# Kernel optimization log

Measured on AMD Instinct MI355X. Metric: run time of the kernel, lower is better.

## Reference

```python
import jax, jax.numpy as jnp
import numpy as np

D = 128          # state dimension d
H = 256          # nabla_V MLP hidden width
NUM_STEPS = 300  # Euler-Maruyama steps
B = 512          # batch of trajectories
T_FINAL = 1.0
LMBD = 1.0


def _mlp(tx, W1, b1, W2, b2):
    # neural_sde.nabla_V : (N, D+1) -> (N, D)
    return jnp.tanh(tx @ W1 + b1) @ W2 + b2


def setup_inputs() -> dict:
    key = jax.random.key(0)
    ks = jax.random.split(key, 8)
    x0 = jax.random.normal(ks[0], (D,), jnp.float32)
    sigma = jnp.eye(D, dtype=jnp.float32)                      # default sigma = I
    A = 0.05 * jax.random.normal(ks[1], (D, D), jnp.float32) - jnp.eye(D)  # stable linear drift b(x)=Ax
    Mp = jax.random.normal(ks[2], (D, D), jnp.float32)
    P = 0.1 * (Mp @ Mp.T) / D
    Mq = jax.random.normal(ks[3], (D, D), jnp.float32)
    Q = 0.1 * (Mq @ Mq.T) / D
    W1 = jax.random.normal(ks[4], (D + 1, H), jnp.float32) / np.sqrt(D + 1)
    b1 = jnp.zeros((H,), jnp.float32)
    W2 = jax.random.normal(ks[5], (H, D), jnp.float32) / np.sqrt(H)
    b2 = jnp.zeros((D,), jnp.float32)
    noises = jax.random.normal(ks[6], (NUM_STEPS, B, D), jnp.float32)  # unit normals
    return dict(x0=x0, sigma=sigma, A=A, P=P, Q=Q, W1=W1, b1=b1, W2=W2, b2=b2, noises=noises)


def reference(x0, sigma, A, P, Q, W1, b1, W2, b2, noises):
    # SOC_Solver.loss(batch_size=B, algorithm='SOCM_const_M')
    ts = jnp.linspace(0.0, T_FINAL, NUM_STEPS + 1)
    dts = ts[1:] - ts[:-1]
    state0 = jnp.broadcast_to(x0, (B, D))

    # ---- utils.stochastic_trajectories: Euler-Maruyama rollout with log-weight accumulation ----
    def step(carry, inp):
        x, lw_det, lw_sto = carry
        t0, dt, noise = inp
        tx = jnp.concatenate([jnp.full((B, 1), t0, x.dtype), x], axis=-1)
        nv = _mlp(tx, W1, b1, W2, b2)
        u = jax.lax.stop_gradient(-nv @ sigma)  # control = -sigma^T nabla_V, detached (SOCM)
        f_val = 0.5 * jnp.einsum('bi,ij,bj->b', x, P, x)
        x_new = x + (x @ A.T + u @ sigma.T) * dt + jnp.sqrt(LMBD * dt) * (noise @ sigma.T)
        lw_det = lw_det + dt * (-0.5 * jnp.sum(u * u, -1) / LMBD - f_val / LMBD)
        lw_sto = lw_sto + jnp.sqrt(dt / LMBD) * jnp.sum(u * noise, -1)
        return (x_new, lw_det, lw_sto), (x_new, u)

    init = (state0, jnp.zeros((B,), state0.dtype), jnp.zeros((B,), state0.dtype))
    (xT, lw_det, lw_sto), (xs, controls) = jax.lax.scan(step, init, (ts[:-1], dts, noises))
    states = jnp.concatenate([state0[None], xs], 0)               # (T+1, B, D)
    log_terminal = -0.5 * jnp.einsum('bi,ij,bj->b', xT, Q, xT) / LMBD
    weight = jnp.exp(lw_det + lw_sto + log_terminal)              # (B,)

    # ---- nabla_V over the whole trajectory ----
    ts_rep = jnp.broadcast_to(ts[:, None, None], (NUM_STEPS + 1, B, 1))
    tx_all = jnp.concatenate([ts_rep, states], -1).reshape(-1, D + 1)
    nabla_V = _mlp(tx_all, W1, b1, W2, b2).reshape(NUM_STEPS + 1, B, D)

    # ---- SOCM_const_M least-squares target ----
    sigma_inv_T = jnp.linalg.inv(sigma).T
    term1 = jnp.einsum('ij,tbj->tbi', P, states[:-1])             # nabla_f(states)[:-1]
    sin_noises = jnp.einsum('ij,tbj->tbi', sigma_inv_T, noises)
    sin_controls = jnp.einsum('ij,tbj->tbi', sigma_inv_T, controls)
    term2 = -jnp.sqrt(LMBD) * jnp.einsum('ij,tbj->tbi', A, sin_noises)   # nabla_b == A (const)
    term3 = -jnp.einsum('ij,tbj->tbi', A, sin_controls)
    target_terminal = states[-1] @ Q.T                            # nabla_g(x_T)

    dt_b = dts[:, None, None]
    z = jnp.zeros((1, B, D), states.dtype)
    t1dt = jnp.concatenate([z, term1 * dt_b], 0)
    t2sdt = jnp.concatenate([z, term2 * jnp.sqrt(dt_b)], 0)
    t3dt = jnp.concatenate([z, term3 * dt_b], 0)
    cs1 = jnp.sum(t1dt, 0, keepdims=True) - jnp.cumsum(t1dt, 0)
    cs2 = jnp.sum(t2sdt, 0, keepdims=True) - jnp.cumsum(t2sdt, 0)
    cs3 = jnp.sum(t3dt, 0, keepdims=True) - jnp.cumsum(t3dt, 0)
    least_squares_target = cs1 + cs2 + cs3 + target_terminal[None]

    control_learned = -jnp.einsum('ij,tbj->tbi', sigma.T, nabla_V)
    control_target = -jnp.einsum('ij,tbj->tbi', sigma.T, least_squares_target)
    w = weight[None, :, None]
    objective = jnp.sum((control_learned - control_target) ** 2 * w) / ((NUM_STEPS + 1) * B)
    return objective
```

## Files before the change

kernel.cpp:

```cpp
#include <hip/hip_runtime.h>
#include <math.h>

#define DD 128
#define HH 256
#define NS 300
#define BB 512
#define NPO (301*64)

__device__ __forceinline__ float tsf(int t){ return (float)((double)t*(1.0/(double)NS)); }

__device__ __forceinline__ float wave_red(float v){
#pragma unroll
  for(int o=32;o>0;o>>=1) v += __shfl_down(v,o);
  return v;
}
__device__ __forceinline__ float fma4(float4 a, float4 b, float acc){
  acc = fmaf(a.x,b.x,acc); acc = fmaf(a.y,b.y,acc);
  acc = fmaf(a.z,b.z,acc); acc = fmaf(a.w,b.w,acc); return acc;
}

__global__ __launch_bounds__(256) void k_pre1(
    const float* __restrict__ sigma,
    float* __restrict__ SIT, float* __restrict__ AUG, int* __restrict__ FLG)
{
  const int j = threadIdx.x;
  __shared__ int s_ok; __shared__ int s_p; __shared__ float s_fac[DD];
  if (j == 0) s_ok = 1;
  __syncthreads();
  bool ok = true;
  for (int idx = j; idx < DD*DD; idx += 256) {
    const int r = idx >> 7, c = idx & 127;
    if (sigma[idx] != (r==c ? 1.f : 0.f)) ok = false;
  }
  if (!ok) s_ok = 0;
  __syncthreads();
  const bool ident = (s_ok != 0);
  if (j == 0) *FLG = ident ? 1 : 0;
  if (ident) {
    for (int idx = j; idx < DD*DD; idx += 256) {
      const int r = idx >> 7, c = idx & 127;
      SIT[idx] = (r==c) ? 1.f : 0.f;
    }
    return;
  }
  for (int idx = j; idx < DD*256; idx += 256) {
    const int r = idx >> 8, c = idx & 255;
    AUG[idx] = (c < DD) ? sigma[r*DD + c] : ((c-DD)==r ? 1.f : 0.f);
  }
  __syncthreads();
  for (int c = 0; c < DD; ++c) {
    if (j == 0) {
      int p = c; float best = fabsf(AUG[c*256 + c]);
      for (int r2 = c+1; r2 < DD; ++r2) {
        const float v = fabsf(AUG[r2*256 + c]);
        if (v > best) { best = v; p = r2; }
      }
      s_p = p;
    }
    __syncthreads();
    const int p = s_p;
    if (p != c) {
      const float tmp = AUG[c*256 + j];
      AUG[c*256 + j] = AUG[p*256 + j];
      AUG[p*256 + j] = tmp;
    }
    __syncthreads();
    const float pd = AUG[c*256 + c];
    const float rowv = AUG[c*256 + j];
    __syncthreads();
    AUG[c*256 + j] = rowv / pd;
    if (j < DD) s_fac[j] = (j == c) ? 0.f : AUG[j*256 + c];
    __syncthreads();
    const float prj = AUG[c*256 + j];
    for (int r2 = 0; r2 < DD; ++r2) {
      if (r2 != c) AUG[r2*256 + j] -= s_fac[r2] * prj;
    }
    __syncthreads();
  }
  for (int idx = j; idx < DD*DD; idx += 256) {
    const int j2 = idx >> 7, k = idx & 127;
    SIT[idx] = AUG[k*256 + DD + j2];
  }
}

__global__ __launch_bounds__(256) void k_pre2(
    const float* __restrict__ W1, const float* __restrict__ W2,
    const float* __restrict__ A, const float* __restrict__ P,
    const float* __restrict__ Q, const float* __restrict__ sigma,
    const float* __restrict__ SIT, const int* __restrict__ FLG,
    float* __restrict__ W1L, float* __restrict__ W2L,
    float* __restrict__ AL, float* __restrict__ PL,
    float* __restrict__ ML, float* __restrict__ SL,
    float* __restrict__ STL, float* __restrict__ QL,
    float* __restrict__ SGC)
{
  const int g = blockIdx.x*256 + threadIdx.x;
  const int gs = gridDim.x*256;
  const bool ident = (*FLG != 0);
  for (int idx = g; idx < 32*256; idx += gs) {
    const int k4 = idx >> 8, hj = idx & 255;
#pragma unroll
    for (int j = 0; j < 4; ++j)
      W1L[idx*4 + j] = W1[(4*k4 + 1 + j)*HH + hj];
  }
  for (int idx = g; idx < 64*128; idx += gs) {
    const int k4 = idx >> 7, i = idx & 127;
#pragma unroll
    for (int j = 0; j < 4; ++j)
      W2L[idx*4 + j] = W2[(4*k4 + j)*DD + i];
  }
  for (int idx = g; idx < 32*128; idx += gs) {
    const int k4 = idx >> 7, i = idx & 127;
#pragma unroll
    for (int j = 0; j < 4; ++j) {
      AL [idx*4 + j] = A[i*DD + 4*k4 + j];
      PL [idx*4 + j] = P[i*DD + 4*k4 + j];
      QL [idx*4 + j] = Q[i*DD + 4*k4 + j];
      STL[idx*4 + j] = sigma[i*DD + 4*k4 + j];
      SL [idx*4 + j] = sigma[(4*k4 + j)*DD + i];
      float m;
      if (ident) m = -A[i*DD + 4*k4 + j];
      else {
        float acc = 0.f;
        for (int jj = 0; jj < DD; ++jj)
          acc = fmaf(A[i*DD + jj], SIT[jj*DD + 4*k4 + j], acc);
        m = -acc;
      }
      ML[idx*4 + j] = m;
    }
  }
  for (int idx = g; idx < DD*DD; idx += gs) {
    const int i2 = idx >> 7, k = idx & 127;
    SGC[idx] = sigma[k*DD + i2];
  }
}

__global__ __launch_bounds__(512) void k_roll_id4(
    const float* __restrict__ x0,
    const float* __restrict__ W1, const float* __restrict__ b1,
    const float* __restrict__ b2, const float* __restrict__ noises,
    const float* __restrict__ W1L, const float* __restrict__ W2L,
    const float* __restrict__ AL, const float* __restrict__ PL,
    const float* __restrict__ QL, const int* __restrict__ FLG,
    float* __restrict__ U, float* __restrict__ TL,
    float* __restrict__ TGT, float* __restrict__ WGT)
{
  if (*FLG == 0) return;
  __shared__ __align__(16) float xs[4][128];
  __shared__ __align__(16) float hs[4][256];
  __shared__ __align__(16) float wv[4][128];
  __shared__ __align__(16) float p2[2][4][256];
  __shared__ __align__(16) float p4[4][4][128];
  __shared__ __align__(16) float pm3[3][4][4][128];
  __shared__ float red[16];

  const float4* W1L4 = (const float4*)W1L;
  const float4* W2L4 = (const float4*)W2L;
  const float4* AL4  = (const float4*)AL;
  const float4* PL4  = (const float4*)PL;
  const float4* QL4  = (const float4*)QL;
  float4* xs4 = (float4*)&xs[0][0];
  float4* hs4 = (float4*)&hs[0][0];
  float4* wv4 = (float4*)&wv[0][0];
  float* p4f = &p4[0][0][0];
  float* pA  = &pm3[0][0][0][0];
  float* pP  = &pm3[1][0][0][0];
  float* pM  = &pm3[2][0][0][0];

  const int tid = threadIdx.x;
  const int hj = tid & 255, hg = tid >> 8;
  const int i  = tid & 127, q  = tid >> 7;
  const int wid = tid >> 6;
  const int b0 = blockIdx.x * 4;
  const float w1t = (hg == 0) ? W1[hj] : 0.f;
  const float b1c = b1[hj];
  const float b2i = b2[i];

  xs[q][i] = x0[i];

  float lwloc = 0.f, u_reg = 0.f, nz = 0.f;

  for (int t = 0; t <= NS; ++t) {
    __syncthreads();
    const float t0 = tsf(t);
    const float dt = tsf(t+1) - t0;
    const float sdt = sqrtf(dt);
    nz = (t < NS) ? noises[((size_t)t*BB + b0 + q)*DD + i] : 0.f;

    {
      float a0 = t0*w1t, a1 = t0*w1t, a2 = t0*w1t, a3 = t0*w1t;
#pragma unroll
      for (int m = 0; m < 16; ++m) {
        const float4 w = W1L4[(hg*16 + m)*256 + hj];
        a0 = fma4(w, xs4[0*32 + hg*16 + m], a0);
        a1 = fma4(w, xs4[1*32 + hg*16 + m], a1);
        a2 = fma4(w, xs4[2*32 + hg*16 + m], a2);
        a3 = fma4(w, xs4[3*32 + hg*16 + m], a3);
      }
      p2[hg][0][hj] = a0; p2[hg][1][hj] = a1;
      p2[hg][2][hj] = a2; p2[hg][3][hj] = a3;
    }
    __syncthreads();
    {
      const int rr = tid >> 8, cc = tid & 255;
      hs[rr][cc]     = tanhf(p2[0][rr][cc]     + p2[1][rr][cc]     + b1c);
      hs[rr + 2][cc] = tanhf(p2[0][rr + 2][cc] + p2[1][rr + 2][cc] + b1c);
    }
    __syncthreads();
    {
      float c0 = 0.f, c1 = 0.f, c2 = 0.f, c3 = 0.f;
#pragma unroll
      for (int m = 0; m < 16; ++m) {
        const float4 w2 = W2L4[(q*16 + m)*128 + i];
        c0 = fma4(w2, hs4[0*64 + q*16 + m], c0);
        c1 = fma4(w2, hs4[1*64 + q*16 + m], c1);
        c2 = fma4(w2, hs4[2*64 + q*16 + m], c2);
        c3 = fma4(w2, hs4[3*64 + q*16 + m], c3);
      }
      p4f[q*512 + 0*128 + i] = c0; p4f[q*512 + 1*128 + i] = c1;
      p4f[q*512 + 2*128 + i] = c2; p4f[q*512 + 3*128 + i] = c3;
    }
    __syncthreads();
    {
      const float nv = p4f[0*512 + q*128 + i] + p4f[1*512 + q*128 + i]
                     + p4f[2*512 + q*128 + i] + p4f[3*512 + q*128 + i] + b2i;
      u_reg = -nv;
      U[((size_t)t*BB + b0 + q)*DD + i] = u_reg;
      if (t < NS) {
        wv[q][i] = sdt*nz + dt*u_reg;
        lwloc += sdt*u_reg*nz - 0.5f*dt*u_reg*u_reg;
      }
    }
    if (t == NS) break;
    __syncthreads();
    {
      float aA[4] = {0,0,0,0}, aP_[4] = {0,0,0,0}, aM[4] = {0,0,0,0};
#pragma unroll
      for (int m = 0; m < 8; ++m) {
        const float4 av = AL4[(q*8 + m)*128 + i];
        const float4 pv = PL4[(q*8 + m)*128 + i];
#pragma unroll
        for (int r = 0; r < 4; ++r) {
          const float4 xv = xs4[r*32 + q*8 + m];
          const float4 wvv = wv4[r*32 + q*8 + m];
          aA[r] = fma4(av, xv, aA[r]);
          aP_[r] = fma4(pv, xv, aP_[r]);
          aM[r] = fma4(av, wvv, aM[r]);
        }
      }
#pragma unroll
      for (int r = 0; r < 4; ++r) {
        pA[q*512 + r*128 + i] = aA[r];
        pP[q*512 + r*128 + i] = aP_[r];
        pM[q*512 + r*128 + i] = aM[r];
      }
    }
    __syncthreads();
    {
      const float xo = xs[q][i];
      const float xa = pA[0*512 + q*128 + i] + pA[1*512 + q*128 + i]
                     + pA[2*512 + q*128 + i] + pA[3*512 + q*128 + i];
      const float yy = pP[0*512 + q*128 + i] + pP[1*512 + q*128 + i]
                     + pP[2*512 + q*128 + i] + pP[3*512 + q*128 + i];
      const float mm = -(pM[0*512 + q*128 + i] + pM[1*512 + q*128 + i]
                       + pM[2*512 + q*128 + i] + pM[3*512 + q*128 + i]);
      TL[(size_t)(t+1)*(BB*DD) + (size_t)(b0 + q)*DD + i] = dt*yy + mm;
      xs[q][i] = xo + (xa + u_reg)*dt + sdt*nz;
      lwloc -= 0.5f*dt*xo*yy;
    }
  }
  __syncthreads();
  {
    float g0 = 0.f, g1 = 0.f, g2 = 0.f, g3 = 0.f;
#pragma unroll
    for (int m = 0; m < 8; ++m) {
      const float4 qv = QL4[(q*8 + m)*128 + i];
      g0 = fma4(qv, xs4[0*32 + q*8 + m], g0);
      g1 = fma4(qv, xs4[1*32 + q*8 + m], g1);
      g2 = fma4(qv, xs4[2*32 + q*8 + m], g2);
      g3 = fma4(qv, xs4[3*32 + q*8 + m], g3);
    }
    pA[q*512 + 0*128 + i] = g0; pA[q*512 + 1*128 + i] = g1;
    pA[q*512 + 2*128 + i] = g2; pA[q*512 + 3*128 + i] = g3;
  }
  __syncthreads();
  float qloc;
  {
    const float tt = pA[0*512 + q*128 + i] + pA[1*512 + q*128 + i]
                   + pA[2*512 + q*128 + i] + pA[3*512 + q*128 + i];
    TGT[(b0 + q)*DD + i] = tt;
    qloc = xs[q][i]*tt;
  }
  const float rq = wave_red(qloc);
  const float rl = wave_red(lwloc);
  if ((tid & 63) == 0) { red[wid] = rq; red[8 + wid] = rl; }
  __syncthreads();
  if (tid < 4) {
    const float qf = red[2*tid] + red[2*tid + 1];
    const float lw = red[8 + 2*tid] + red[8 + 2*tid + 1];
    WGT[b0 + tid] = expf(lw - 0.5f*qf);
  }
}

__global__ __launch_bounds__(512) void k_roll_gen(
    const float* __restrict__ x0,
    const float* __restrict__ W1, const float* __restrict__ b1,
    const float* __restrict__ b2, const float* __restrict__ noises,
    const float* __restrict__ W1L, const float* __restrict__ W2L,
    const float* __restrict__ AL, const float* __restrict__ PL,
    const float* __restrict__ ML, const float* __restrict__ SL,
    const float* __restrict__ STL, const float* __restrict__ QL,
    const int* __restrict__ FLG,
    float* __restrict__ U, float* __restrict__ TL,
    float* __restrict__ TGT, float* __restrict__ WGT)
{
  if (*FLG != 0) return;
  __shared__ __align__(16) float xs[2][128];
  __shared__ __align__(16) float hs[2][256];
  __shared__ __align__(16) float noi[2][128];
  __shared__ __align__(16) float nvs[2][128];
  __shared__ __align__(16) float uu[2][128];
  __shared__ __align__(16) float wv[2][128];
  __shared__ __align__(16) float p2[2][2][256];
  __shared__ __align__(16) float p4[4][2][128];
  __shared__ __align__(16) float pm3[3][4][2][128];
  __shared__ float red[16];

  const float4* W1L4 = (const float4*)W1L;
  const float4* W2L4 = (const float4*)W2L;
  const float4* AL4  = (const float4*)AL;
  const float4* PL4  = (const float4*)PL;
  const float4* ML4  = (const float4*)ML;
  const float4* SL4  = (const float4*)SL;
  const float4* STL4 = (const float4*)STL;
  const float4* QL4  = (const float4*)QL;
  float4* xs4  = (float4*)&xs[0][0];
  float4* hs4  = (float4*)&hs[0][0];
  float4* wv4  = (float4*)&wv[0][0];
  float4* nvs4 = (float4*)&nvs[0][0];
  float4* uu4  = (float4*)&uu[0][0];
  float4* noi4 = (float4*)&noi[0][0];
  float* p2f = &p2[0][0][0];
  float* p4f = &p4[0][0][0];
  float* pA  = &pm3[0][0][0][0];
  float* pP  = &pm3[1][0][0][0];
  float* pM  = &pm3[2][0][0][0];

  const int tid = threadIdx.x;
  const int hj = tid & 255, hg = tid >> 8;
  const int i  = tid & 127, q  = tid >> 7;
  const int wid = tid >> 6;
  const int b0 = blockIdx.x * 2;
  const float w1t = (hg == 0) ? W1[hj] : 0.f;
  const float b1c = b1[hj];
  const float b2i = b2[i];

  if (tid < 256) xs[tid >> 7][tid & 127] = x0[tid & 127];

  float lwloc = 0.f, u_reg = 0.f, nz = 0.f;

  for (int t = 0; t <= NS; ++t) {
    __syncthreads();
    const float t0 = tsf(t);
    const float dt = tsf(t+1) - t0;
    const float sdt = sqrtf(dt);
    nz = 0.f;
    if (q < 2 && t < NS) {
      nz = noises[((size_t)t*BB + b0 + q)*DD + i];
      noi[q][i] = nz;
    }
    {
      float a0 = t0*w1t, a1 = t0*w1t;
#pragma unroll
      for (int m = 0; m < 16; ++m) {
        const float4 w = W1L4[(hg*16 + m)*256 + hj];
        a0 = fma4(w, xs4[hg*16 + m], a0);
        a1 = fma4(w, xs4[32 + hg*16 + m], a1);
      }
      p2[hg][0][hj] = a0; p2[hg][1][hj] = a1;
    }
    __syncthreads();
    {
      const int rr = tid >> 8, cc = tid & 255;
      hs[rr][cc] = tanhf(p2[0][rr][cc] + p2[1][rr][cc] + b1c);
    }
    __syncthreads();
    {
      float c0 = 0.f, c1 = 0.f;
#pragma unroll
      for (int m = 0; m < 16; ++m) {
        const float4 w2 = W2L4[(q*16 + m)*128 + i];
        c0 = fma4(w2, hs4[q*16 + m], c0);
        c1 = fma4(w2, hs4[64 + q*16 + m], c1);
      }
      p4[q][0][i] = c0; p4[q][1][i] = c1;
    }
    __syncthreads();
    if (q < 2) {
      nvs[q][i] = p4[0][q][i] + p4[1][q][i] + p4[2][q][i] + p4[3][q][i] + b2i;
    }
    __syncthreads();
    {
      float s0 = 0.f, s1 = 0.f;
#pragma unroll
      for (int m = 0; m < 8; ++m) {
        const float4 gv = SL4[(q*8 + m)*128 + i];
        s0 = fma4(gv, nvs4[q*8 + m], s0);
        s1 = fma4(gv, nvs4[32 + q*8 + m], s1);
      }
      pA[q*256 + i] = s0; pA[q*256 + 128 + i] = s1;
    }
    __syncthreads();
    if (q < 2) {
      u_reg = -(pA[q*128 + i] + pA[256 + q*128 + i]
              + pA[512 + q*128 + i] + pA[768 + q*128 + i]);
      uu[q][i] = u_reg;
      U[((size_t)t*BB + b0 + q)*DD + i] = u_reg;
      wv[q][i] = sdt*nz + dt*u_reg;
      if (t < NS) lwloc += sdt*u_reg*nz - 0.5f*dt*u_reg*u_reg;
    }
    if (t == NS) break;
    __syncthreads();
    {
      float aA0=0,aA1=0,aP0=0,aP1=0,aM0=0,aM1=0;
#pragma unroll
      for (int m = 0; m < 8; ++m) {
        const float4 av = AL4[(q*8 + m)*128 + i];
        const float4 pv = PL4[(q*8 + m)*128 + i];
        const float4 mv = ML4[(q*8 + m)*128 + i];
        const float4 x0v = xs4[q*8 + m];
        const float4 x1v = xs4[32 + q*8 + m];
        const float4 w0v = wv4[q*8 + m];
        const float4 w1v = wv4[32 + q*8 + m];
        aA0 = fma4(av, x0v, aA0); aA1 = fma4(av, x1v, aA1);
        aP0 = fma4(pv, x0v, aP0); aP1 = fma4(pv, x1v, aP1);
        aM0 = fma4(mv, w0v, aM0); aM1 = fma4(mv, w1v, aM1);
      }
      pA[q*256 + i] = aA0; pA[q*256 + 128 + i] = aA1;
      pP[q*256 + i] = aP0; pP[q*256 + 128 + i] = aP1;
      pM[q*256 + i] = aM0; pM[q*256 + 128 + i] = aM1;
      float su0=0,su1=0,sn0=0,sn1=0;
#pragma unroll
      for (int m = 0; m < 8; ++m) {
        const float4 sv = STL4[(q*8 + m)*128 + i];
        su0 = fma4(sv, uu4[q*8 + m],  su0);
        su1 = fma4(sv, uu4[32 + q*8 + m], su1);
        sn0 = fma4(sv, noi4[q*8 + m], sn0);
        sn1 = fma4(sv, noi4[32 + q*8 + m], sn1);
      }
      p2f[q*256 + i] = su0; p2f[q*256 + 128 + i] = su1;
      p4f[q*256 + i] = sn0; p4f[q*256 + 128 + i] = sn1;
    }
    __syncthreads();
    if (q < 2) {
      const float xo = xs[q][i];
      const float xa = pA[q*128+i] + pA[256+q*128+i] + pA[512+q*128+i] + pA[768+q*128+i];
      const float yy = pP[q*128+i] + pP[256+q*128+i] + pP[512+q*128+i] + pP[768+q*128+i];
      const float mm = pM[q*128+i] + pM[256+q*128+i] + pM[512+q*128+i] + pM[768+q*128+i];
      const float usv = p2f[q*128+i] + p2f[256+q*128+i] + p2f[512+q*128+i] + p2f[768+q*128+i];
      const float nsv = p4f[q*128+i] + p4f[256+q*128+i] + p4f[512+q*128+i] + p4f[768+q*128+i];
      TL[(size_t)(t+1)*(BB*DD) + (size_t)(b0 + q)*DD + i] = dt*yy + mm;
      xs[q][i] = xo + (xa + usv)*dt + sdt*nsv;
      lwloc -= 0.5f*dt*xo*yy;
    }
  }
  __syncthreads();
  {
    float g0 = 0.f, g1 = 0.f;
#pragma unroll
    for (int m = 0; m < 8; ++m) {
      const float4 qv = QL4[(q*8 + m)*128 + i];
      g0 = fma4(qv, xs4[q*8 + m], g0);
      g1 = fma4(qv, xs4[32 + q*8 + m], g1);
    }
    pA[q*256 + i] = g0; pA[q*256 + 128 + i] = g1;
  }
  __syncthreads();
  float qloc = 0.f;
  if (q < 2) {
    const float tt = pA[q*128+i] + pA[256+q*128+i] + pA[512+q*128+i] + pA[768+q*128+i];
    TGT[(b0 + q)*DD + i] = tt;
    qloc = xs[q][i]*tt;
  }
  const float rq = wave_red(qloc);
  const float rl = wave_red(lwloc);
  if ((tid & 63) == 0) { red[wid] = rq; red[8 + wid] = rl; }
  __syncthreads();
  if (tid < 2) {
    const float qf = red[2*tid] + red[2*tid + 1];
    const float lw = red[8 + 2*tid] + red[8 + 2*tid + 1];
    WGT[b0 + tid] = expf(lw - 0.5f*qf);
  }
}

__global__ __launch_bounds__(256) void k_scan(
    const float* __restrict__ TGT, const float* __restrict__ WGT,
    const float* __restrict__ U, float* __restrict__ TL,
    const int* __restrict__ FLG, float* __restrict__ PART_S)
{
  const int tid = threadIdx.x;
  const int bi = blockIdx.x*256 + tid;
  const int b = bi >> 7;
  const bool id = (*FLG != 0);
  const float w = WGT[b];
  float lst = TGT[bi];
  float obj = 0.f;
  if (id) { const float d = lst + U[(size_t)NS*(BB*DD) + bi]; obj = w*d*d; }
#pragma unroll 4
  for (int t = NS; t >= 1; --t) {
    const float v = TL[(size_t)t*(BB*DD) + bi];
    if (!id) TL[(size_t)t*(BB*DD) + bi] = lst;
    lst += v;
    if (id) { const float d = lst + U[(size_t)(t-1)*(BB*DD) + bi]; obj += w*d*d; }
  }
  if (!id) TL[bi] = lst;
  __shared__ float r4[4];
  const float s = wave_red(obj);
  if ((tid & 63) == 0) r4[tid >> 6] = s;
  __syncthreads();
  if (tid == 0) PART_S[blockIdx.x] = id ? (r4[0]+r4[1]+r4[2]+r4[3]) : 0.f;
}

__global__ __launch_bounds__(256) void k_obj(
    const float* __restrict__ SGC, const float* __restrict__ TL,
    const float* __restrict__ U, const float* __restrict__ WGT,
    const int* __restrict__ FLG, float* __restrict__ PART_O)
{
  const int blk = blockIdx.x;
  if (*FLG != 0) { if (threadIdx.x == 0) PART_O[blk] = 0.f; return; }
  const int t = blk >> 6, bg = blk & 63;
  __shared__ __align__(16) float ls[8][132];
  __shared__ __align__(16) float us[8][128];
  __shared__ __align__(16) float pD[2][8][128];
  __shared__ float wg[8];
  __shared__ float r4[4];
  const int tid = threadIdx.x;
  const int i = tid & 127, h = tid >> 7;
  for (int idx = tid; idx < 8*128; idx += 256) {
    const int rr = idx >> 7, k = idx & 127;
    ls[rr][k] = TL[(size_t)t*(BB*DD) + (size_t)(bg*8+rr)*DD + k];
    us[rr][k] = U [(size_t)t*(BB*DD) + (size_t)(bg*8+rr)*DD + k];
  }
  if (tid < 8) wg[tid] = WGT[bg*8 + tid];
  __syncthreads();
  const float* grow = SGC + i*DD + h*64;
#pragma unroll
  for (int rr = 0; rr < 8; ++rr) {
    float a = 0.f;
#pragma unroll
    for (int it = 0; it < 16; ++it) {
      float4 gv = *(const float4*)(grow + it*4);
      float4 l4 = *(const float4*)&ls[rr][h*64 + it*4];
      a = fma4(gv, l4, a);
    }
    pD[h][rr][i] = a;
  }
  __syncthreads();
  float obj = 0.f;
#pragma unroll
  for (int p = 0; p < 4; ++p) {
    const int rr = h*4 + p;
    const float d = pD[0][rr][i] + pD[1][rr][i] + us[rr][i];
    obj += wg[rr]*d*d;
  }
  const float s = wave_red(obj);
  if ((tid & 63) == 0) r4[tid >> 6] = s;
  __syncthreads();
  if (tid == 0) PART_O[blk] = r4[0]+r4[1]+r4[2]+r4[3];
}

__global__ __launch_bounds__(256) void k_fin(
    const float* __restrict__ PART_S, const float* __restrict__ PART_O,
    float* __restrict__ out)
{
  const int tid = threadIdx.x;
  float s = PART_S[tid];
  for (int idx = tid; idx < NPO; idx += 256) s += PART_O[idx];
  __shared__ float r4[4];
  const float v = wave_red(s);
  if ((tid & 63) == 0) r4[tid >> 6] = v;
  __syncthreads();
  if (tid == 0) out[0] = (r4[0]+r4[1]+r4[2]+r4[3]) * (1.0f/((float)(NS+1)*(float)BB));
}

extern "C" void kernel_launch(void* const* d_in, const int* in_sizes, int n_in,
                              void* d_out, int out_size, void* d_ws, size_t ws_size,
                              hipStream_t stream) {
  (void)in_sizes; (void)n_in; (void)out_size; (void)ws_size;
  const float* x0     = (const float*)d_in[0];
  const float* sigma  = (const float*)d_in[1];
  const float* A      = (const float*)d_in[2];
  const float* P      = (const float*)d_in[3];
  const float* Q      = (const float*)d_in[4];
  const float* W1     = (const float*)d_in[5];
  const float* b1     = (const float*)d_in[6];
  const float* W2     = (const float*)d_in[7];
  const float* b2     = (const float*)d_in[8];
  const float* noises = (const float*)d_in[9];

  float* ws = (float*)d_ws;
  const size_t SL_ = (size_t)BB*DD;
  float* TL     = ws;
  float* U      = TL + (size_t)(NS+1)*SL_;
  float* TGT    = U  + (size_t)(NS+1)*SL_;
  float* WGT    = TGT + SL_;
  float* W1Lw   = WGT + BB;
  float* W2Lw   = W1Lw + 32*256*4;
  float* ALm    = W2Lw + 64*128*4;
  float* PLm    = ALm + 32*128*4;
  float* MLm    = PLm + 32*128*4;
  float* SLm    = MLm + 32*128*4;
  float* STLm   = SLm + 32*128*4;
  float* QLm    = STLm + 32*128*4;
  float* SGC    = QLm + 32*128*4;
  float* SIT    = SGC + (size_t)DD*DD;
  float* AUG    = SIT + (size_t)DD*DD;
  float* PART_S = AUG + (size_t)DD*256;
  float* PART_O = PART_S + 256;
  int*   FLG    = (int*)(PART_O + NPO);
  float* out    = (float*)d_out;

  k_pre1<<<1, 256, 0, stream>>>(sigma, SIT, AUG, FLG);
  k_pre2<<<64, 256, 0, stream>>>(W1, W2, A, P, Q, sigma, SIT, FLG,
                                 W1Lw, W2Lw, ALm, PLm, MLm, SLm, STLm, QLm, SGC);
  k_roll_id4<<<128, 512, 0, stream>>>(x0, W1, b1, b2, noises,
                                      W1Lw, W2Lw, ALm, PLm, QLm, FLG,
                                      U, TL, TGT, WGT);
  k_roll_gen<<<256, 512, 0, stream>>>(x0, W1, b1, b2, noises,
                                      W1Lw, W2Lw, ALm, PLm, MLm, SLm, STLm, QLm,
                                      FLG, U, TL, TGT, WGT);
  k_scan<<<(BB*DD)/256, 256, 0, stream>>>(TGT, WGT, U, TL, FLG, PART_S);
  k_obj<<<NPO, 256, 0, stream>>>(SGC, TL, U, WGT, FLG, PART_O);
  k_fin<<<1, 256, 0, stream>>>(PART_S, PART_O, out);
}
```

Baseline: 1.821 ms.

## Process eight trajectories per block in identity-sigma rollout kernel

After: 4.591 ms. 2.52x slower.

```diff
diff --git a/kernel.cpp b/kernel.cpp
--- a/kernel.cpp
+++ b/kernel.cpp
@@ -6,6 +6,16 @@
 #define NS 300
 #define BB 512
 #define NPO (301*64)
+
+#define I8_XS   0
+#define I8_HS   1024
+#define I8_WV   3072
+#define I8_P2   4096
+#define I8_P4   8192
+#define I8_PM3  12288
+#define I8_RED  24576
+#define I8_FLOATS 24608
+#define I8_BYTES (I8_FLOATS*4)
 
 __device__ __forceinline__ float tsf(int t){ return (float)((double)t*(1.0/(double)NS)); }
 
@@ -135,7 +145,7 @@
   }
 }
 
-__global__ __launch_bounds__(512) void k_roll_id4(
+__global__ __launch_bounds__(512) void k_roll_id8(
     const float* __restrict__ x0,
     const float* __restrict__ W1, const float* __restrict__ b1,
     const float* __restrict__ b2, const float* __restrict__ noises,
@@ -146,159 +156,198 @@
     float* __restrict__ TGT, float* __restrict__ WGT)
 {
   if (*FLG == 0) return;
-  __shared__ __align__(16) float xs[4][128];
-  __shared__ __align__(16) float hs[4][256];
-  __shared__ __align__(16) float wv[4][128];
-  __shared__ __align__(16) float p2[2][4][256];
-  __shared__ __align__(16) float p4[4][4][128];
-  __shared__ __align__(16) float pm3[3][4][4][128];
-  __shared__ float red[16];
-
+  extern __shared__ float sm[];
+  float*  xs  = sm + I8_XS;
+  float*  hs  = sm + I8_HS;
+  float*  wv  = sm + I8_WV;
+  float*  p2  = sm + I8_P2;
+  float*  p4f = sm + I8_P4;
+  float*  pm3 = sm + I8_PM3;
+  float*  red = sm + I8_RED;
+  float4* xs4 = (float4*)xs;
+  float4* hs4 = (float4*)hs;
+  float4* wv4 = (float4*)wv;
+  float*  pA = pm3, *pP = pm3 + 4096, *pM = pm3 + 8192;
   const float4* W1L4 = (const float4*)W1L;
   const float4* W2L4 = (const float4*)W2L;
   const float4* AL4  = (const float4*)AL;
   const float4* PL4  = (const float4*)PL;
   const float4* QL4  = (const float4*)QL;
-  float4* xs4 = (float4*)&xs[0][0];
-  float4* hs4 = (float4*)&hs[0][0];
-  float4* wv4 = (float4*)&wv[0][0];
-  float* p4f = &p4[0][0][0];
-  float* pA  = &pm3[0][0][0][0];
-  float* pP  = &pm3[1][0][0][0];
-  float* pM  = &pm3[2][0][0][0];
 
   const int tid = threadIdx.x;
   const int hj = tid & 255, hg = tid >> 8;
   const int i  = tid & 127, q  = tid >> 7;
   const int wid = tid >> 6;
-  const int b0 = blockIdx.x * 4;
+  const int b0 = blockIdx.x * 8;
   const float w1t = (hg == 0) ? W1[hj] : 0.f;
   const float b1c = b1[hj];
   const float b2i = b2[i];
 
-  xs[q][i] = x0[i];
-
-  float lwloc = 0.f, u_reg = 0.f, nz = 0.f;
+  xs[q*128 + i] = x0[i];
+  xs[(q + 4)*128 + i] = x0[i];
+
+  float lw0 = 0.f, lw1 = 0.f;
+  float u0 = 0.f, u1 = 0.f, nz0 = 0.f, nz1 = 0.f;
 
   for (int t = 0; t <= NS; ++t) {
     __syncthreads();
     const float t0 = tsf(t);
     const float dt = tsf(t+1) - t0;
     const float sdt = sqrtf(dt);
-    nz = (t < NS) ? noises[((size_t)t*BB + b0 + q)*DD + i] : 0.f;
-
-    {
-      float a0 = t0*w1t, a1 = t0*w1t, a2 = t0*w1t, a3 = t0*w1t;
+    if (t < NS) {
+      nz0 = noises[((size_t)t*BB + b0 + q)*DD + i];
+      nz1 = noises[((size_t)t*BB + b0 + q + 4)*DD + i];
+    } else { nz0 = 0.f; nz1 = 0.f; }
+
+    {
+      float a[8];
+#pragma unroll
+      for (int r = 0; r < 8; ++r) a[r] = t0*w1t;
 #pragma unroll
       for (int m = 0; m < 16; ++m) {
         const float4 w = W1L4[(hg*16 + m)*256 + hj];
-        a0 = fma4(w, xs4[0*32 + hg*16 + m], a0);
-        a1 = fma4(w, xs4[1*32 + hg*16 + m], a1);
-        a2 = fma4(w, xs4[2*32 + hg*16 + m], a2);
-        a3 = fma4(w, xs4[3*32 + hg*16 + m], a3);
-      }
-      p2[hg][0][hj] = a0; p2[hg][1][hj] = a1;
-      p2[hg][2][hj] = a2; p2[hg][3][hj] = a3;
-    }
-    __syncthreads();
-    {
-      const int rr = tid >> 8, cc = tid & 255;
-      hs[rr][cc]     = tanhf(p2[0][rr][cc]     + p2[1][rr][cc]     + b1c);
-      hs[rr + 2][cc] = tanhf(p2[0][rr + 2][cc] + p2[1][rr + 2][cc] + b1c);
-    }
-    __syncthreads();
-    {
-      float c0 = 0.f, c1 = 0.f, c2 = 0.f, c3 = 0.f;
+#pragma unroll
+        for (int r = 0; r < 8; ++r)
+          a[r] = fma4(w, xs4[r*32 + hg*16 + m], a[r]);
+      }
+#pragma unroll
+      for (int r = 0; r < 8; ++r) p2[hg*2048 + r*256 + hj] = a[r];
+    }
+    __syncthreads();
+    {
+#pragma unroll
+      for (int rr = 0; rr < 4; ++rr) {
+        const int r = hg + rr*2;
+        hs[r*256 + hj] = tanhf(p2[r*256 + hj] + p2[2048 + r*256 + hj] + b1c);
+      }
+    }
+    __syncthreads();
+    {
+      float c[8];
+#pragma unroll
+      for (int r = 0; r < 8; ++r) c[r] = 0.f;
 #pragma unroll
       for (int m = 0; m < 16; ++m) {
         const float4 w2 = W2L4[(q*16 + m)*128 + i];
-        c0 = fma4(w2, hs4[0*64 + q*16 + m], c0);
-        c1 = fma4(w2, hs4[1*64 + q*16 + m], c1);
-        c2 = fma4(w2, hs4[2*64 + q*16 + m], c2);
-        c3 = fma4(w2, hs4[3*64 + q*16 + m], c3);
-      }
-      p4f[q*512 + 0*128 + i] = c0; p4f[q*512 + 1*128 + i] = c1;
-      p4f[q*512 + 2*128 + i] = c2; p4f[q*512 + 3*128 + i] = c3;
-    }
-    __syncthreads();
-    {
-      const float nv = p4f[0*512 + q*128 + i] + p4f[1*512 + q*128 + i]
-                     + p4f[2*512 + q*128 + i] + p4f[3*512 + q*128 + i] + b2i;
-      u_reg = -nv;
-      U[((size_t)t*BB + b0 + q)*DD + i] = u_reg;
+#pragma unroll
+        for (int r = 0; r < 8; ++r)
+          c[r] = fma4(w2, hs4[r*64 + q*16 + m], c[r]);
+      }
+#pragma unroll
+      for (int r = 0; r < 8; ++r) p4f[q*1024 + r*128 + i] = c[r];
+    }
+    __syncthreads();
+    {
+      const int r0 = q, r1 = q + 4;
+      const float nv0 = p4f[0*1024 + r0*128 + i] + p4f[1*1024 + r0*128 + i]
+                      + p4f[2*1024 + r0*128 + i] + p4f[3*1024 + r0*128 + i] + b2i;
+      const float nv1 = p4f[0*1024 + r1*128 + i] + p4f[1*1024 + r1*128 + i]
+                      + p4f[2*1024 + r1*128 + i] + p4f[3*1024 + r1*128 + i] + b2i;
+      u0 = -nv0; u1 = -nv1;
+      U[((size_t)t*BB + b0 + r0)*DD + i] = u0;
+      U[((size_t)t*BB + b0 + r1)*DD + i] = u1;
       if (t < NS) {
-        wv[q][i] = sdt*nz + dt*u_reg;
-        lwloc += sdt*u_reg*nz - 0.5f*dt*u_reg*u_reg;
+        wv[r0*128 + i] = sdt*nz0 + dt*u0;
+        wv[r1*128 + i] = sdt*nz1 + dt*u1;
+        lw0 += sdt*u0*nz0 - 0.5f*dt*u0*u0;
+        lw1 += sdt*u1*nz1 - 0.5f*dt*u1*u1;
       }
     }
     if (t == NS) break;
     __syncthreads();
     {
-      float aA[4] = {0,0,0,0}, aP_[4] = {0,0,0,0}, aM[4] = {0,0,0,0};
+      float aA[8], aP_[8], aM[8];
+#pragma unroll
+      for (int r = 0; r < 8; ++r) { aA[r] = 0.f; aP_[r] = 0.f; aM[r] = 0.f; }
 #pragma unroll
       for (int m = 0; m < 8; ++m) {
         const float4 av = AL4[(q*8 + m)*128 + i];
         const float4 pv = PL4[(q*8 + m)*128 + i];
 #pragma unroll
-        for (int r = 0; r < 4; ++r) {
-          const float4 xv = xs4[r*32 + q*8 + m];
+        for (int r = 0; r < 8; ++r) {
+          const float4 xv  = xs4[r*32 + q*8 + m];
           const float4 wvv = wv4[r*32 + q*8 + m];
-          aA[r] = fma4(av, xv, aA[r]);
+          aA[r]  = fma4(av, xv, aA[r]);
           aP_[r] = fma4(pv, xv, aP_[r]);
-          aM[r] = fma4(av, wvv, aM[r]);
+          aM[r]  = fma4(av, wvv, aM[r]);
         }
       }
 #pragma unroll
-      for (int r = 0; r < 4; ++r) {
-        pA[q*512 + r*128 + i] = aA[r];
-        pP[q*512 + r*128 + i] = aP_[r];
-        pM[q*512 + r*128 + i] = aM[r];
-      }
-    }
-    __syncthreads();
-    {
-      const float xo = xs[q][i];
-      const float xa = pA[0*512 + q*128 + i] + pA[1*512 + q*128 + i]
-                     + pA[2*512 + q*128 + i] + pA[3*512 + q*128 + i];
-      const float yy = pP[0*512 + q*128 + i] + pP[1*512 + q*128 + i]
-                     + pP[2*512 + q*128 + i] + pP[3*512 + q*128 + i];
-      const float mm = -(pM[0*512 + q*128 + i] + pM[1*512 + q*128 + i]
-                       + pM[2*512 + q*128 + i] + pM[3*512 + q*128 + i]);
-      TL[(size_t)(t+1)*(BB*DD) + (size_t)(b0 + q)*DD + i] = dt*yy + mm;
-      xs[q][i] = xo + (xa + u_reg)*dt + sdt*nz;
-      lwloc -= 0.5f*dt*xo*yy;
+      for (int r = 0; r < 8; ++r) {
+        pA[q*1024 + r*128 + i] = aA[r];
+        pP[q*1024 + r*128 + i] = aP_[r];
+        pM[q*1024 + r*128 + i] = aM[r];
+      }
+    }
+    __syncthreads();
+    {
+#pragma unroll
+      for (int p = 0; p < 2; ++p) {
+        const int r = q + 4*p;
+        const float u_r = (p == 0) ? u0 : u1;
+        const float nz_r = (p == 0) ? nz0 : nz1;
+        const float xo = xs[r*128 + i];
+        const float xa = pA[0*1024 + r*128 + i] + pA[1*1024 + r*128 + i]
+                       + pA[2*1024 + r*128 + i] + pA[3*1024 + r*128 + i];
+        const float yy = pP[0*1024 + r*128 + i] + pP[1*1024 + r*128 + i]
+                       + pP[2*1024 + r*128 + i] + pP[3*1024 + r*128 + i];
+        const float mm = -(pM[0*1024 + r*128 + i] + pM[1*1024 + r*128 + i]
+                         + pM[2*1024 + r*128 + i] + pM[3*1024 + r*128 + i]);
+        TL[(size_t)(t+1)*(BB*DD) + (size_t)(b0 + r)*DD + i] = dt*yy + mm;
+        xs[r*128 + i] = xo + (xa + u_r)*dt + sdt*nz_r;
+        if (p == 0) lw0 -= 0.5f*dt*xo*yy; else lw1 -= 0.5f*dt*xo*yy;
+      }
     }
   }
   __syncthreads();
   {
-    float g0 = 0.f, g1 = 0.f, g2 = 0.f, g3 = 0.f;
+    float g[8];
+#pragma unroll
+    for (int r = 0; r < 8; ++r) g[r] = 0.f;
 #pragma unroll
     for (int m = 0; m < 8; ++m) {
       const float4 qv = QL4[(q*8 + m)*128 + i];
-      g0 = fma4(qv, xs4[0*32 + q*8 + m], g0);
-      g1 = fma4(qv, xs4[1*32 + q*8 + m], g1);
-      g2 = fma4(qv, xs4[2*32 + q*8 + m], g2);
-      g3 = fma4(qv, xs4[3*32 + q*8 + m], g3);
-    }
-    pA[q*512 + 0*128 + i] = g0; pA[q*512 + 1*128 + i] = g1;
-    pA[q*512 + 2*128 + i] = g2; pA[q*512 + 3*128 + i] = g3;
-  }
-  __syncthreads();
-  float qloc;
+#pragma unroll
+      for (int r = 0; r < 8; ++r)
+        g[r] = fma4(qv, xs4[r*32 + q*8 + m], g[r]);
+    }
+#pragma unroll
+    for (int r = 0; r < 8; ++r) pA[q*1024 + r*128 + i] = g[r];
+  }
+  __syncthreads();
+  float q0 = 0.f, q1 = 0.f;
   {
-    const float tt = pA[0*512 + q*128 + i] + pA[1*512 + q*128 + i]
-                   + pA[2*512 + q*128 + i] + pA[3*512 + q*128 + i];
-    TGT[(b0 + q)*DD + i] = tt;
-    qloc = xs[q][i]*tt;
-  }
-  const float rq = wave_red(qloc);
-  const float rl = wave_red(lwloc);
-  if ((tid & 63) == 0) { red[wid] = rq; red[8 + wid] = rl; }
-  __syncthreads();
-  if (tid < 4) {
-    const float qf = red[2*tid] + red[2*tid + 1];
-    const float lw = red[8 + 2*tid] + red[8 + 2*tid + 1];
-    WGT[b0 + tid] = expf(lw - 0.5f*qf);
+    const int r0 = q, r1 = q + 4;
+    const float tt0 = pA[0*1024 + r0*128 + i] + pA[1*1024 + r0*128 + i]
+                    + pA[2*1024 + r0*128 + i] + pA[3*1024 + r0*128 + i];
+    const float tt1 = pA[0*1024 + r1*128 + i] + pA[1*1024 + r1*128 + i]
+                    + pA[2*1024 + r1*128 + i] + pA[3*1024 + r1*128 + i];
+    TGT[(b0 + r0)*DD + i] = tt0;
+    TGT[(b0 + r1)*DD + i] = tt1;
+    q0 = xs[r0*128 + i]*tt0;
+    q1 = xs[r1*128 + i]*tt1;
+  }
+  const float rq0 = wave_red(q0);
+  const float rq1 = wave_red(q1);
+  const float rl0 = wave_red(lw0);
+  const float rl1 = wave_red(lw1);
+  if ((tid & 63) == 0) {
+    red[wid] = rq0; red[8 + wid] = rq1;
+    red[16 + wid] = rl0; red[24 + wid] = rl1;
+  }
+  __syncthreads();
+  if (tid < 8) {
+    const int r = tid;
+    float qf, lw;
+    if (r < 4) {
+      qf = red[2*r] + red[2*r + 1];
+      lw = red[16 + 2*r] + red[16 + 2*r + 1];
+    } else {
+      const int r2 = r - 4;
+      qf = red[8 + 2*r2] + red[8 + 2*r2 + 1];
+      lw = red[24 + 2*r2] + red[24 + 2*r2 + 1];
+    }
+    WGT[b0 + r] = expf(lw - 0.5f*qf);
   }
 }
 
@@ -620,12 +669,15 @@
   int*   FLG    = (int*)(PART_O + NPO);
   float* out    = (float*)d_out;
 
+  (void)hipFuncSetAttribute((const void*)k_roll_id8,
+                            hipFuncAttributeMaxDynamicSharedMemorySize, I8_BYTES);
+
   k_pre1<<<1, 256, 0, stream>>>(sigma, SIT, AUG, FLG);
   k_pre2<<<64, 256, 0, stream>>>(W1, W2, A, P, Q, sigma, SIT, FLG,
                                  W1Lw, W2Lw, ALm, PLm, MLm, SLm, STLm, QLm, SGC);
-  k_roll_id4<<<128, 512, 0, stream>>>(x0, W1, b1, b2, noises,
-                                      W1Lw, W2Lw, ALm, PLm, QLm, FLG,
-                                      U, TL, TGT, WGT);
+  k_roll_id8<<<64, 512, I8_BYTES, stream>>>(x0, W1, b1, b2, noises,
+                                            W1Lw, W2Lw, ALm, PLm, QLm, FLG,
+                                            U, TL, TGT, WGT);
   k_roll_gen<<<256, 512, 0, stream>>>(x0, W1, b1, b2, noises,
                                       W1Lw, W2Lw, ALm, PLm, MLm, SLm, STLm, QLm,
                                       FLG, U, TL, TGT, WGT);
```

## Fold A into W2 to merge rollout phases and cut per-step barriers

Applied to the files above, without the earlier changes.

Result: slower. 3.355 ms (+84.2%).

```diff
diff --git a/kernel.cpp b/kernel.cpp
--- a/kernel.cpp
+++ b/kernel.cpp
@@ -87,11 +87,13 @@
     const float* __restrict__ W1, const float* __restrict__ W2,
     const float* __restrict__ A, const float* __restrict__ P,
     const float* __restrict__ Q, const float* __restrict__ sigma,
-    const float* __restrict__ SIT, const int* __restrict__ FLG,
+    const float* __restrict__ b2, const float* __restrict__ SIT,
+    const int* __restrict__ FLG,
     float* __restrict__ W1L, float* __restrict__ W2L,
     float* __restrict__ AL, float* __restrict__ PL,
     float* __restrict__ ML, float* __restrict__ SL,
     float* __restrict__ STL, float* __restrict__ QL,
+    float* __restrict__ W2ATL, float* __restrict__ Ab2,
     float* __restrict__ SGC)
 {
   const int g = blockIdx.x*256 + threadIdx.x;
@@ -129,43 +131,60 @@
       ML[idx*4 + j] = m;
     }
   }
+  for (int idx = g; idx < 64*128; idx += gs) {
+    const int k4 = idx >> 7, i2 = idx & 127;
+    const float4* arow = (const float4*)(A + (size_t)i2*DD);
+#pragma unroll
+    for (int j = 0; j < 4; ++j) {
+      const float4* wrow = (const float4*)(W2 + (size_t)(4*k4 + j)*DD);
+      float acc = 0.f;
+      for (int m = 0; m < 32; ++m) acc = fma4(wrow[m], arow[m], acc);
+      W2ATL[idx*4 + j] = acc;
+    }
+  }
+  for (int idx = g; idx < DD; idx += gs) {
+    float acc = 0.f;
+    for (int k = 0; k < DD; ++k) acc = fmaf(A[idx*DD + k], b2[k], acc);
+    Ab2[idx] = acc;
+  }
   for (int idx = g; idx < DD*DD; idx += gs) {
     const int i2 = idx >> 7, k = idx & 127;
     SGC[idx] = sigma[k*DD + i2];
   }
 }
 
-__global__ __launch_bounds__(512) void k_roll_id4(
+__global__ __launch_bounds__(512) void k_roll_id4w(
     const float* __restrict__ x0,
     const float* __restrict__ W1, const float* __restrict__ b1,
     const float* __restrict__ b2, const float* __restrict__ noises,
     const float* __restrict__ W1L, const float* __restrict__ W2L,
-    const float* __restrict__ AL, const float* __restrict__ PL,
-    const float* __restrict__ QL, const int* __restrict__ FLG,
+    const float* __restrict__ W2ATL, const float* __restrict__ AL,
+    const float* __restrict__ PL, const float* __restrict__ QL,
+    const float* __restrict__ Ab2, const int* __restrict__ FLG,
     float* __restrict__ U, float* __restrict__ TL,
     float* __restrict__ TGT, float* __restrict__ WGT)
 {
   if (*FLG == 0) return;
   __shared__ __align__(16) float xs[4][128];
   __shared__ __align__(16) float hs[4][256];
-  __shared__ __align__(16) float wv[4][128];
+  __shared__ __align__(16) float noi[4][128];
   __shared__ __align__(16) float p2[2][4][256];
-  __shared__ __align__(16) float p4[4][4][128];
-  __shared__ __align__(16) float pm3[3][4][4][128];
+  __shared__ __align__(16) float pNv[4][4][128];
+  __shared__ __align__(16) float pNa[4][4][128];
+  __shared__ __align__(16) float pAx[4][4][128];
+  __shared__ __align__(16) float pPx[4][4][128];
+  __shared__ __align__(16) float pNz[4][4][128];
   __shared__ float red[16];
 
   const float4* W1L4 = (const float4*)W1L;
   const float4* W2L4 = (const float4*)W2L;
+  const float4* WAT4 = (const float4*)W2ATL;
   const float4* AL4  = (const float4*)AL;
   const float4* PL4  = (const float4*)PL;
   const float4* QL4  = (const float4*)QL;
-  float4* xs4 = (float4*)&xs[0][0];
-  float4* hs4 = (float4*)&hs[0][0];
-  float4* wv4 = (float4*)&wv[0][0];
-  float* p4f = &p4[0][0][0];
-  float* pA  = &pm3[0][0][0][0];
-  float* pP  = &pm3[1][0][0][0];
-  float* pM  = &pm3[2][0][0][0];
+  float4* xs4  = (float4*)&xs[0][0];
+  float4* hs4  = (float4*)&hs[0][0];
+  float4* noi4 = (float4*)&noi[0][0];
 
   const int tid = threadIdx.x;
   const int hj = tid & 255, hg = tid >> 8;
@@ -175,17 +194,18 @@
   const float w1t = (hg == 0) ? W1[hj] : 0.f;
   const float b1c = b1[hj];
   const float b2i = b2[i];
+  const float ab2i = Ab2[i];
 
   xs[q][i] = x0[i];
-
-  float lwloc = 0.f, u_reg = 0.f, nz = 0.f;
+  noi[q][i] = noises[(size_t)(b0 + q)*DD + i];
+
+  float lwloc = 0.f;
 
   for (int t = 0; t <= NS; ++t) {
     __syncthreads();
     const float t0 = tsf(t);
     const float dt = tsf(t+1) - t0;
     const float sdt = sqrtf(dt);
-    nz = (t < NS) ? noises[((size_t)t*BB + b0 + q)*DD + i] : 0.f;
 
     {
       float a0 = t0*w1t, a1 = t0*w1t, a2 = t0*w1t, a3 = t0*w1t;
@@ -200,41 +220,8 @@
       p2[hg][0][hj] = a0; p2[hg][1][hj] = a1;
       p2[hg][2][hj] = a2; p2[hg][3][hj] = a3;
     }
-    __syncthreads();
-    {
-      const int rr = tid >> 8, cc = tid & 255;
-      hs[rr][cc]     = tanhf(p2[0][rr][cc]     + p2[1][rr][cc]     + b1c);
-      hs[rr + 2][cc] = tanhf(p2[0][rr + 2][cc] + p2[1][rr + 2][cc] + b1c);
-    }
-    __syncthreads();
-    {
-      float c0 = 0.f, c1 = 0.f, c2 = 0.f, c3 = 0.f;
-#pragma unroll
-      for (int m = 0; m < 16; ++m) {
-        const float4 w2 = W2L4[(q*16 + m)*128 + i];
-        c0 = fma4(w2, hs4[0*64 + q*16 + m], c0);
-        c1 = fma4(w2, hs4[1*64 + q*16 + m], c1);
-        c2 = fma4(w2, hs4[2*64 + q*16 + m], c2);
-        c3 = fma4(w2, hs4[3*64 + q*16 + m], c3);
-      }
-      p4f[q*512 + 0*128 + i] = c0; p4f[q*512 + 1*128 + i] = c1;
-      p4f[q*512 + 2*128 + i] = c2; p4f[q*512 + 3*128 + i] = c3;
-    }
-    __syncthreads();
-    {
-      const float nv = p4f[0*512 + q*128 + i] + p4f[1*512 + q*128 + i]
-                     + p4f[2*512 + q*128 + i] + p4f[3*512 + q*128 + i] + b2i;
-      u_reg = -nv;
-      U[((size_t)t*BB + b0 + q)*DD + i] = u_reg;
-      if (t < NS) {
-        wv[q][i] = sdt*nz + dt*u_reg;
-        lwloc += sdt*u_reg*nz - 0.5f*dt*u_reg*u_reg;
-      }
-    }
-    if (t == NS) break;
-    __syncthreads();
-    {
-      float aA[4] = {0,0,0,0}, aP_[4] = {0,0,0,0}, aM[4] = {0,0,0,0};
+    {
+      float ax[4] = {0,0,0,0}, an[4] = {0,0,0,0}, py[4] = {0,0,0,0};
 #pragma unroll
       for (int m = 0; m < 8; ++m) {
         const float4 av = AL4[(q*8 + m)*128 + i];
@@ -242,52 +229,91 @@
 #pragma unroll
         for (int r = 0; r < 4; ++r) {
           const float4 xv = xs4[r*32 + q*8 + m];
-          const float4 wvv = wv4[r*32 + q*8 + m];
-          aA[r] = fma4(av, xv, aA[r]);
-          aP_[r] = fma4(pv, xv, aP_[r]);
-          aM[r] = fma4(av, wvv, aM[r]);
+          const float4 nv = noi4[r*32 + q*8 + m];
+          ax[r] = fma4(av, xv, ax[r]);
+          an[r] = fma4(av, nv, an[r]);
+          py[r] = fma4(pv, xv, py[r]);
         }
       }
 #pragma unroll
       for (int r = 0; r < 4; ++r) {
-        pA[q*512 + r*128 + i] = aA[r];
-        pP[q*512 + r*128 + i] = aP_[r];
-        pM[q*512 + r*128 + i] = aM[r];
-      }
-    }
-    __syncthreads();
-    {
-      const float xo = xs[q][i];
-      const float xa = pA[0*512 + q*128 + i] + pA[1*512 + q*128 + i]
-                     + pA[2*512 + q*128 + i] + pA[3*512 + q*128 + i];
-      const float yy = pP[0*512 + q*128 + i] + pP[1*512 + q*128 + i]
-                     + pP[2*512 + q*128 + i] + pP[3*512 + q*128 + i];
-      const float mm = -(pM[0*512 + q*128 + i] + pM[1*512 + q*128 + i]
-                       + pM[2*512 + q*128 + i] + pM[3*512 + q*128 + i]);
-      TL[(size_t)(t+1)*(BB*DD) + (size_t)(b0 + q)*DD + i] = dt*yy + mm;
-      xs[q][i] = xo + (xa + u_reg)*dt + sdt*nz;
-      lwloc -= 0.5f*dt*xo*yy;
-    }
+        pAx[q][r][i] = ax[r];
+        pNz[q][r][i] = an[r];
+        pPx[q][r][i] = py[r];
+      }
+    }
+    __syncthreads();
+    {
+#pragma unroll
+      for (int rr = 0; rr < 2; ++rr) {
+        const int r = hg + 2*rr;
+        hs[r][hj] = tanhf(p2[0][r][hj] + p2[1][r][hj] + b1c);
+      }
+    }
+    __syncthreads();
+    {
+      float c[4] = {0,0,0,0}, d[4] = {0,0,0,0};
+#pragma unroll
+      for (int m = 0; m < 16; ++m) {
+        const float4 w2 = W2L4[(q*16 + m)*128 + i];
+        const float4 wa = WAT4[(q*16 + m)*128 + i];
+#pragma unroll
+        for (int r = 0; r < 4; ++r) {
+          const float4 hv = hs4[r*64 + q*16 + m];
+          c[r] = fma4(w2, hv, c[r]);
+          d[r] = fma4(wa, hv, d[r]);
+        }
+      }
+#pragma unroll
+      for (int r = 0; r < 4; ++r) {
+        pNv[q][r][i] = c[r];
+        pNa[q][r][i] = d[r];
+      }
+    }
+    __syncthreads();
+    {
+      const float nv = pNv[0][q][i] + pNv[1][q][i]
+                     + pNv[2][q][i] + pNv[3][q][i] + b2i;
+      const float u_reg = -nv;
+      U[((size_t)t*BB + b0 + q)*DD + i] = u_reg;
+      if (t < NS) {
+        const float nvA = pNa[0][q][i] + pNa[1][q][i]
+                        + pNa[2][q][i] + pNa[3][q][i];
+        const float anz = pNz[0][q][i] + pNz[1][q][i]
+                        + pNz[2][q][i] + pNz[3][q][i];
+        const float xa  = pAx[0][q][i] + pAx[1][q][i]
+                        + pAx[2][q][i] + pAx[3][q][i];
+        const float yy  = pPx[0][q][i] + pPx[1][q][i]
+                        + pPx[2][q][i] + pPx[3][q][i];
+        const float nz = noi[q][i];
+        const float mm = -sdt*anz + dt*(nvA + ab2i);
+        TL[(size_t)(t+1)*(BB*DD) + (size_t)(b0 + q)*DD + i] = dt*yy + mm;
+        const float xo = xs[q][i];
+        xs[q][i] = xo + (xa + u_reg)*dt + sdt*nz;
+        lwloc += sdt*u_reg*nz - dt*(0.5f*u_reg*u_reg + 0.5f*xo*yy);
+        if (t + 1 < NS)
+          noi[q][i] = noises[((size_t)(t+1)*BB + b0 + q)*DD + i];
+      }
+    }
+    if (t == NS) break;
   }
   __syncthreads();
   {
-    float g0 = 0.f, g1 = 0.f, g2 = 0.f, g3 = 0.f;
+    float g[4] = {0,0,0,0};
 #pragma unroll
     for (int m = 0; m < 8; ++m) {
       const float4 qv = QL4[(q*8 + m)*128 + i];
-      g0 = fma4(qv, xs4[0*32 + q*8 + m], g0);
-      g1 = fma4(qv, xs4[1*32 + q*8 + m], g1);
-      g2 = fma4(qv, xs4[2*32 + q*8 + m], g2);
-      g3 = fma4(qv, xs4[3*32 + q*8 + m], g3);
-    }
-    pA[q*512 + 0*128 + i] = g0; pA[q*512 + 1*128 + i] = g1;
-    pA[q*512 + 2*128 + i] = g2; pA[q*512 + 3*128 + i] = g3;
+#pragma unroll
+      for (int r = 0; r < 4; ++r)
+        g[r] = fma4(qv, xs4[r*32 + q*8 + m], g[r]);
+    }
+#pragma unroll
+    for (int r = 0; r < 4; ++r) pAx[q][r][i] = g[r];
   }
   __syncthreads();
   float qloc;
   {
-    const float tt = pA[0*512 + q*128 + i] + pA[1*512 + q*128 + i]
-                   + pA[2*512 + q*128 + i] + pA[3*512 + q*128 + i];
+    const float tt = pAx[0][q][i] + pAx[1][q][i] + pAx[2][q][i] + pAx[3][q][i];
     TGT[(b0 + q)*DD + i] = tt;
     qloc = xs[q][i]*tt;
   }
@@ -612,7 +638,9 @@
   float* SLm    = MLm + 32*128*4;
   float* STLm   = SLm + 32*128*4;
   float* QLm    = STLm + 32*128*4;
-  float* SGC    = QLm + 32*128*4;
+  float* W2ATLw = QLm + 32*128*4;
+  float* Ab2w   = W2ATLw + 64*128*4;
+  float* SGC    = Ab2w + DD;
   float* SIT    = SGC + (size_t)DD*DD;
   float* AUG    = SIT + (size_t)DD*DD;
   float* PART_S = AUG + (size_t)DD*256;
@@ -621,11 +649,12 @@
   float* out    = (float*)d_out;
 
   k_pre1<<<1, 256, 0, stream>>>(sigma, SIT, AUG, FLG);
-  k_pre2<<<64, 256, 0, stream>>>(W1, W2, A, P, Q, sigma, SIT, FLG,
-                                 W1Lw, W2Lw, ALm, PLm, MLm, SLm, STLm, QLm, SGC);
-  k_roll_id4<<<128, 512, 0, stream>>>(x0, W1, b1, b2, noises,
-                                      W1Lw, W2Lw, ALm, PLm, QLm, FLG,
-                                      U, TL, TGT, WGT);
+  k_pre2<<<256, 256, 0, stream>>>(W1, W2, A, P, Q, sigma, b2, SIT, FLG,
+                                  W1Lw, W2Lw, ALm, PLm, MLm, SLm, STLm, QLm,
+                                  W2ATLw, Ab2w, SGC);
+  k_roll_id4w<<<128, 512, 0, stream>>>(x0, W1, b1, b2, noises,
+                                       W1Lw, W2Lw, W2ATLw, ALm, PLm, QLm,
+                                       Ab2w, FLG, U, TL, TGT, WGT);
   k_roll_gen<<<256, 512, 0, stream>>>(x0, W1, b1, b2, noises,
                                       W1Lw, W2Lw, ALm, PLm, MLm, SLm, STLm, QLm,
                                       FLG, U, TL, TGT, WGT);
```
